# Performance work log

Hardware: AMD Instinct MI355X
Metric: run time of the kernel (lower is better)

The kernel has to match this reference:

```python
import jax, jax.numpy as jnp
import numpy as np

WIN_SIZE = 11
SIGMA = 1.5
WEIGHTS = np.array([0.0448, 0.2856, 0.3001, 0.2363, 0.1333], dtype=np.float32)
K1, K2 = 0.01, 0.03
DATA_RANGE = 255.0
C1 = (K1 * DATA_RANGE) ** 2
C2 = (K2 * DATA_RANGE) ** 2
N_SCALES = 5


def _gauss1d():
    coords = np.arange(WIN_SIZE, dtype=np.float32) - WIN_SIZE // 2
    g = np.exp(-(coords ** 2) / (2.0 * SIGMA ** 2))
    g /= g.sum()
    return jnp.asarray(g, dtype=jnp.float32)


def _blur(x, g):
    # separable depthwise gaussian blur, VALID padding (matches pytorch_msssim)
    C = x.shape[1]
    wh = jnp.tile(g.reshape(1, 1, 1, WIN_SIZE), (C, 1, 1, 1))
    wv = jnp.tile(g.reshape(1, 1, WIN_SIZE, 1), (C, 1, 1, 1))
    dn = ('NCHW', 'OIHW', 'NCHW')
    x = jax.lax.conv_general_dilated(x, wh, (1, 1), 'VALID', dimension_numbers=dn, feature_group_count=C)
    x = jax.lax.conv_general_dilated(x, wv, (1, 1), 'VALID', dimension_numbers=dn, feature_group_count=C)
    return x


def _ssim(X, Y, g):
    mu1 = _blur(X, g)
    mu2 = _blur(Y, g)
    mu1_sq = mu1 * mu1
    mu2_sq = mu2 * mu2
    mu1_mu2 = mu1 * mu2
    sigma1_sq = _blur(X * X, g) - mu1_sq
    sigma2_sq = _blur(Y * Y, g) - mu2_sq
    sigma12 = _blur(X * Y, g) - mu1_mu2
    cs_map = (2.0 * sigma12 + C2) / (sigma1_sq + sigma2_sq + C2)
    ssim_map = ((2.0 * mu1_mu2 + C1) / (mu1_sq + mu2_sq + C1)) * cs_map
    return ssim_map.mean(axis=(2, 3)), cs_map.mean(axis=(2, 3))  # [B,C] each


def _avg_pool2(x):
    # avg_pool2d kernel=2 stride=2; H,W chosen even at every scale so padding=0
    return jax.lax.reduce_window(x, 0.0, jax.lax.add, (1, 1, 2, 2), (1, 1, 2, 2), 'VALID') / 4.0


def setup_inputs() -> dict:
    key = jax.random.key(0)
    k1, k2 = jax.random.split(key)
    shape = (32, 3, 384, 384)
    prediction = jax.random.uniform(k1, shape, dtype=jnp.float32) * DATA_RANGE
    truth = jax.random.uniform(k2, shape, dtype=jnp.float32) * DATA_RANGE
    return {"prediction": prediction, "truth": truth}


def reference(prediction, truth):
    g = _gauss1d()
    w = jnp.asarray(WEIGHTS)
    X, Y = prediction, truth
    mcs = []
    for i in range(N_SCALES):
        ssim_pc, cs = _ssim(X, Y, g)
        if i < N_SCALES - 1:
            mcs.append(jax.nn.relu(cs))
            X = _avg_pool2(X)
            Y = _avg_pool2(Y)
    vals = jnp.stack(mcs + [jax.nn.relu(ssim_pc)], axis=0)  # [5,B,C]
    ms_ssim_val = jnp.prod(vals ** w.reshape(-1, 1, 1), axis=0)  # [B,C]
    return 1.0 - ms_ssim_val.mean()
```

## Files before the change

kernel.cpp:

```cpp
#include <hip/hip_runtime.h>
#include <math.h>


namespace {

constexpr int NIMG = 96;
constexpr float TWO_C1 = 13.005f;
constexpr float TWO_C2 = 117.045f;

__device__ constexpr float GW[11] = {
    0.00102838f, 0.00759875f, 0.03600077f, 0.10936070f, 0.21300553f,
    0.26601172f,
    0.21300553f, 0.10936070f, 0.03600077f, 0.00759875f, 0.00102838f};

typedef float f2 __attribute__((ext_vector_type(2)));
typedef float f4 __attribute__((ext_vector_type(4)));

__device__ __forceinline__ f2 pk_mul(f2 a, f2 b) {
  f2 d;
  asm("v_pk_mul_f32 %0, %1, %2" : "=v"(d) : "v"(a), "v"(b));
  return d;
}
__device__ __forceinline__ f2 pk_mul_s1lo(f2 a, f2 b) {
  f2 d;
  asm("v_pk_mul_f32 %0, %1, %2 op_sel:[0,0] op_sel_hi:[1,0]"
      : "=v"(d) : "v"(a), "v"(b));
  return d;
}
__device__ __forceinline__ void fma_w(f2& d, f2 q, f2 p) {
  asm("v_pk_fma_f32 %0, %1, %2, %0 op_sel:[0,0,0] op_sel_hi:[0,1,1]"
      : "+v"(d) : "v"(q), "v"(p));
}
__device__ __forceinline__ void fma_nl(f2& d, f2 q, f2 t) {
  asm("v_pk_fma_f32 %0, %1, %2, %0 op_sel:[0,0,0] op_sel_hi:[1,0,1]"
      : "+v"(d) : "v"(q), "v"(t));
}
__device__ __forceinline__ void fma_nh(f2& d, f2 q, f2 t) {
  asm("v_pk_fma_f32 %0, %1, %2, %0 op_sel:[0,1,0] op_sel_hi:[1,1,1]"
      : "+v"(d) : "v"(q), "v"(t));
}
__device__ __forceinline__ void fma_sl(f2& d, f2 q, f2 t) {
  asm("v_pk_fma_f32 %0, %1, %2, %0 op_sel:[1,0,0] op_sel_hi:[0,0,1]"
      : "+v"(d) : "v"(q), "v"(t));
}
__device__ __forceinline__ void fma_sh(f2& d, f2 q, f2 t) {
  asm("v_pk_fma_f32 %0, %1, %2, %0 op_sel:[1,1,0] op_sel_hi:[0,1,1]"
      : "+v"(d) : "v"(q), "v"(t));
}

__device__ __forceinline__ float wshl1(float v) {
  return __int_as_float(__builtin_amdgcn_mov_dpp(
      __float_as_int(v), 0x130, 0xF, 0xF, true));
}
__device__ __forceinline__ f2 wshl1v(f2 v) {
  f2 r;
  r.x = wshl1(v.x);
  r.y = wshl1(v.y);
  return r;
}

struct SPtrs {
  const float* x0;
  const float* y0;
  const float* ip[4];
};

template <bool BASE, bool CLAMP>
__device__ __forceinline__ void vblur(const float* __restrict__ XP,
                                      const float* __restrict__ YP, int row0,
                                      int W2, int H, int cp, f2 (&AU)[4],
                                      f2 (&AW)[4], f2 (&BU)[4], f2 (&BW)[4],
                                      const f2 (&QQ)[6]) {
  const f2* PA = (const f2*)XP;
  const f2* PB = (const f2*)YP;
  const f4* PV = (const f4*)XP;
  f2 sa[14], sb[14];
  f4 sv[14];
#pragma unroll
  for (int j = 0; j < 14; ++j) {
    int rin = row0 + j;
    if (CLAMP) rin = rin < H - 1 ? rin : H - 1;
    const int off = rin * W2 + cp;
    if (BASE) {
      sa[j] = PA[off];
      sb[j] = PB[off];
    } else {
      sv[j] = PV[off];
    }
  }
  __builtin_amdgcn_sched_barrier(0);
#pragma unroll
  for (int j = 0; j < 14; ++j) {
    f2 Pu, Pw;
    if (BASE) {
      f2 pa = sa[j], pb = sb[j];
      Pu = pa + pb;
      Pw = pa - pb;
    } else {
      f4 v = sv[j];
      Pu.x = v.x; Pu.y = v.y;
      Pw.x = v.z; Pw.y = v.w;
    }
    f2 Qu = pk_mul(Pu, Pu), Qw = pk_mul(Pw, Pw);
#pragma unroll
    for (int i = 0; i < 4; ++i) {
      const int k = j - i;
      if (k >= 0 && k <= 10) {
        const int qi = k <= 5 ? k : 10 - k;
        fma_w(AU[i], QQ[qi], Pu);
        fma_w(AW[i], QQ[qi], Pw);
        fma_w(BU[i], QQ[qi], Qu);
        fma_w(BW[i], QQ[qi], Qw);
      }
    }
  }
}

__global__ __launch_bounds__(256, 3) void ssim_all(SPtrs sp,
                                                   float* __restrict__ acc) {
  __shared__ float red[2][4];

  const int tile = blockIdx.x;
  int s;
  if (tile < 96) s = 0;
  else if (tile < 120) s = 1;
  else if (tile < 126) s = 2;
  else if (tile < 129) s = 3;
  else s = 4;
  const int tstart[5] = {0, 96, 120, 126, 129};
  const int HH[5] = {384, 192, 96, 48, 24};
  const int NTX[5] = {4, 2, 1, 1, 1};
  const int TWM[5] = {94, 92, 86, 38, 14};
  const int lt = tile - tstart[s];
  const int H = HH[s], W = H, OH = H - 10, OW = W - 10, W2 = W >> 1;
  const int tx = lt % NTX[s], by = lt / NTX[s];
  const int x0 = tx * TWM[s];
  const int tw = (TWM[s] < OW - x0) ? TWM[s] : OW - x0;
  const int img = blockIdx.z;

  const float* XP;
  const float* YP = nullptr;
  if (s == 0) {
    XP = sp.x0 + (size_t)img * 384 * 384;
    YP = sp.y0 + (size_t)img * 384 * 384;
  } else {
    XP = sp.ip[s - 1] + (size_t)img * H * W * 2;
  }

  const int t = threadIdx.x;
  const int lane = t & 63, wv = t >> 6;
  int cp = (x0 >> 1) + lane;
  cp = cp < W2 - 1 ? cp : W2 - 1;
  const int row0 = by * 16 + wv * 4;

  f2 QQ[6];
  QQ[0].x = GW[0]; QQ[0].y = 0.f;
#pragma unroll
  for (int n = 1; n < 6; ++n) { QQ[n].x = GW[n]; QQ[n].y = GW[n - 1]; }

  float ssim_s = 0.f, cs_s = 0.f;

  if (row0 < OH) {
    f2 AU[4] = {}, AW[4] = {}, BU[4] = {}, BW[4] = {};
    const bool noclamp = (row0 + 13 <= H - 1);
    if (s == 0) {
      if (noclamp) vblur<true, false>(XP, YP, row0, W2, H, cp, AU, AW, BU, BW, QQ);
      else         vblur<true, true >(XP, YP, row0, W2, H, cp, AU, AW, BU, BW, QQ);
    } else {
      if (noclamp) vblur<false, false>(XP, YP, row0, W2, H, cp, AU, AW, BU, BW, QQ);
      else         vblur<false, true >(XP, YP, row0, W2, H, cp, AU, AW, BU, BW, QQ);
    }

    auto hb = [&QQ](f2 tt) -> f2 {
      f2 h = pk_mul_s1lo(QQ[0], tt);
      fma_nh(h, QQ[1], tt);
      tt = wshl1v(tt);
      fma_nl(h, QQ[2], tt);
      fma_nh(h, QQ[3], tt);
      tt = wshl1v(tt);
      fma_nl(h, QQ[4], tt);
      fma_nh(h, QQ[5], tt);
      tt = wshl1v(tt);
      fma_sl(h, QQ[5], tt);
      fma_sh(h, QQ[4], tt);
      tt = wshl1v(tt);
      fma_sl(h, QQ[3], tt);
      fma_sh(h, QQ[2], tt);
      tt = wshl1v(tt);
      fma_sl(h, QQ[1], tt);
      fma_sh(h, QQ[0], tt);
      return h;
    };

    const bool vx = (2 * lane) < tw;
    const bool vy = (2 * lane + 1) < tw;
#pragma unroll
    for (int i = 0; i < 4; ++i) {
      if (row0 + i < OH) {
        f2 bU = hb(AU[i]), bW = hb(AW[i]);
        f2 bU2 = hb(BU[i]), bW2 = hb(BW[i]);
        f2 m2u = pk_mul(bU, bU), m2w = pk_mul(bW, bW);
        f2 Pm = m2u - m2w;
        f2 Qm = m2u + m2w;
        f2 Am = bU2 - bW2;
        f2 Bm = bU2 + bW2;
        float csx = (Am.x - Pm.x + TWO_C2) *
                    __builtin_amdgcn_rcpf(Bm.x - Qm.x + TWO_C2);
        float lx = (Pm.x + TWO_C1) * __builtin_amdgcn_rcpf(Qm.x + TWO_C1);
        float csy = (Am.y - Pm.y + TWO_C2) *
                    __builtin_amdgcn_rcpf(Bm.y - Qm.y + TWO_C2);
        float ly = (Pm.y + TWO_C1) * __builtin_amdgcn_rcpf(Qm.y + TWO_C1);
        if (vx) { cs_s += csx; ssim_s += lx * csx; }
        if (vy) { cs_s += csy; ssim_s += ly * csy; }
      }
    }
  }

#pragma unroll
  for (int off = 32; off > 0; off >>= 1) {
    ssim_s += __shfl_down(ssim_s, off);
    cs_s += __shfl_down(cs_s, off);
  }
  if (lane == 0) { red[0][wv] = ssim_s; red[1][wv] = cs_s; }
  __syncthreads();
  if (t == 0) {
    atomicAdd(&acc[(2 * s + 0) * NIMG + img],
              red[0][0] + red[0][1] + red[0][2] + red[0][3]);
    atomicAdd(&acc[(2 * s + 1) * NIMG + img],
              red[1][0] + red[1][1] + red[1][2] + red[1][3]);
  }
}

__global__ __launch_bounds__(256) void pyramid_kernel(
    const float* __restrict__ X, const float* __restrict__ Y,
    float* __restrict__ i1, float* __restrict__ i2,
    float* __restrict__ i3, float* __restrict__ i4,
    float* __restrict__ acc) {
  const int img = blockIdx.y;
  const int t = threadIdx.x;
  if (blockIdx.x == 0 && img == 0) {
    for (int i = t; i < 10 * NIMG; i += 256) acc[i] = 0.f;
  }
  const int wv = t >> 6, lane = t & 63;
  const int tidx = blockIdx.x * 4 + wv;
  const int tx = tidx % 6, ty = tidx / 6;
  const int r = lane >> 4, c = lane & 15;

  const float* Xs = X + (size_t)img * 384 * 384;
  const float* Ys = Y + (size_t)img * 384 * 384;
  f4* p1 = (f4*)i1 + (size_t)img * 192 * 96;
  f4* p2 = (f4*)i2 + (size_t)img * 96 * 48;
  f4* p3 = (f4*)i3 + (size_t)img * 48 * 24;
  f4* p4 = (f4*)i4 + (size_t)img * 24 * 12;

  float h4u = 0.f, h4w = 0.f;
#pragma unroll
  for (int b = 0; b < 2; ++b) {
    const int gr = ty * 16 + b * 8 + 2 * r;
    const int gc = tx * 64 + 4 * c;
    f4 xu = *(const f4*)&Xs[(size_t)gr * 384 + gc];
    f4 xv = *(const f4*)&Xs[(size_t)(gr + 1) * 384 + gc];
    f4 yu = *(const f4*)&Ys[(size_t)gr * 384 + gc];
    f4 yv = *(const f4*)&Ys[(size_t)(gr + 1) * 384 + gc];
    float ax = 0.25f * (xu.x + xu.y + xv.x + xv.y);
    float bx = 0.25f * (xu.z + xu.w + xv.z + xv.w);
    float ay = 0.25f * (yu.x + yu.y + yv.x + yv.y);
    float by = 0.25f * (yu.z + yu.w + yv.z + yv.w);
    float u0 = ax + ay, u1v = bx + by, w0 = ax - ay, w1v = bx - by;
    {
      f4 st; st.x = u0; st.y = u1v; st.z = w0; st.w = w1v;
      p1[(size_t)(ty * 8 + b * 4 + r) * 96 + tx * 16 + c] = st;
    }
    float hu = u0 + u1v, hw = w0 + w1v;
    float su = 0.25f * (hu + __shfl_xor(hu, 16));
    float sw = 0.25f * (hw + __shfl_xor(hw, 16));
    float suh = __shfl_xor(su, 1), swh = __shfl_xor(sw, 1);
    if ((r & 1) == 0 && (c & 1) == 0) {
      f4 st; st.x = su; st.y = suh; st.z = sw; st.w = swh;
      p2[(size_t)(ty * 4 + 2 * b + (r >> 1)) * 48 + tx * 8 + (c >> 1)] = st;
    }
    float au = su + __shfl_xor(su, 1);
    float aw = sw + __shfl_xor(sw, 1);
    float u3 = 0.25f * (au + __shfl_xor(au, 32));
    float w3 = 0.25f * (aw + __shfl_xor(aw, 32));
    float u3h = __shfl_xor(u3, 2), w3h = __shfl_xor(w3, 2);
    if (r == 0 && (c & 3) == 0) {
      f4 st; st.x = u3; st.y = u3h; st.z = w3; st.w = w3h;
      p3[(size_t)(ty * 2 + b) * 24 + tx * 4 + (c >> 2)] = st;
    }
    float hu4 = u3 + __shfl_xor(u3, 2);
    float hw4 = w3 + __shfl_xor(w3, 2);
    if (b == 0) {
      h4u = hu4; h4w = hw4;
    } else {
      float l4u = 0.25f * (h4u + hu4), l4w = 0.25f * (h4w + hw4);
      float l4uh = __shfl_xor(l4u, 4), l4wh = __shfl_xor(l4w, 4);
      if (r == 0 && (c & 7) == 0) {
        f4 st; st.x = l4u; st.y = l4uh; st.z = l4w; st.w = l4wh;
        p4[(size_t)ty * 12 + tx * 2 + (c >> 3)] = st;
      }
    }
  }
}

__global__ void final_kernel(const float* __restrict__ acc,
                             float* __restrict__ out) {
  __shared__ float prods[NIMG];
  const float wts[5] = {0.0448f, 0.2856f, 0.3001f, 0.2363f, 0.1333f};
  const float inv_npix[5] = {1.f / (374.f * 374.f), 1.f / (182.f * 182.f),
                             1.f / (86.f * 86.f),  1.f / (38.f * 38.f),
                             1.f / (14.f * 14.f)};
  int t = threadIdx.x;
  if (t < NIMG) {
    float p = 1.f;
#pragma unroll
    for (int s = 0; s < 5; ++s) {
      float sum = (s < 4) ? acc[(s * 2 + 1) * NIMG + t]
                          : acc[(s * 2 + 0) * NIMG + t];
      float m = sum * inv_npix[s];
      m = m > 0.f ? m : 0.f;
      p *= powf(m, wts[s]);
    }
    prods[t] = p;
  }
  __syncthreads();
  if (t == 0) {
    float s = 0.f;
    for (int i = 0; i < NIMG; ++i) s += prods[i];
    out[0] = 1.f - s / (float)NIMG;
  }
}

}

extern "C" void kernel_launch(void* const* d_in, const int* in_sizes, int n_in,
                              void* d_out, int out_size, void* d_ws,
                              size_t ws_size, hipStream_t stream) {
  const float* X0 = (const float*)d_in[0];
  const float* Y0 = (const float*)d_in[1];
  float* out = (float*)d_out;
  float* ws = (float*)d_ws;

  const size_t L1 = (size_t)NIMG * 192 * 192 * 2;
  const size_t L2 = (size_t)NIMG * 96 * 96 * 2;
  const size_t L3 = (size_t)NIMG * 48 * 48 * 2;
  const size_t L4 = (size_t)NIMG * 24 * 24 * 2;

  float* i1 = ws;
  float* i2 = i1 + L1;
  float* i3 = i2 + L2;
  float* i4 = i3 + L3;
  float* acc = i4 + L4;

  pyramid_kernel<<<dim3(36, NIMG), dim3(256), 0, stream>>>(
      X0, Y0, i1, i2, i3, i4, acc);

  SPtrs sp;
  sp.x0 = X0; sp.y0 = Y0;
  sp.ip[0] = i1; sp.ip[1] = i2; sp.ip[2] = i3; sp.ip[3] = i4;

  ssim_all<<<dim3(130, 1, NIMG), dim3(256), 0, stream>>>(sp, acc);

  final_kernel<<<dim3(1), dim3(128), 0, stream>>>(acc, out);
}
```

Measured before the change: 232.8 us.

## Stage block's input rows in shared memory and raise occupancy target

Each block now cooperatively loads its 26 input rows (the 16-row tile plus the 10-row halo) into LDS as sum/difference pairs once, and each wave reads its 14 rows from LDS. Previously every wave fetched its own 14 rows from global memory, so overlapping halo rows were loaded several times. The launch bound is raised from 3 to 6 blocks per SIMD to improve latency hiding. In exchange this adds a __syncthreads and LDS traffic, and the tighter register budget may cause spills. The pyramid offset expression is also rewritten to an equivalent form.

```diff
diff --git a/kernel.cpp b/kernel.cpp
--- a/kernel.cpp
+++ b/kernel.cpp
@@ -65,59 +65,10 @@
   const float* ip[4];
 };
 
-template <bool BASE, bool CLAMP>
-__device__ __forceinline__ void vblur(const float* __restrict__ XP,
-                                      const float* __restrict__ YP, int row0,
-                                      int W2, int H, int cp, f2 (&AU)[4],
-                                      f2 (&AW)[4], f2 (&BU)[4], f2 (&BW)[4],
-                                      const f2 (&QQ)[6]) {
-  const f2* PA = (const f2*)XP;
-  const f2* PB = (const f2*)YP;
-  const f4* PV = (const f4*)XP;
-  f2 sa[14], sb[14];
-  f4 sv[14];
-#pragma unroll
-  for (int j = 0; j < 14; ++j) {
-    int rin = row0 + j;
-    if (CLAMP) rin = rin < H - 1 ? rin : H - 1;
-    const int off = rin * W2 + cp;
-    if (BASE) {
-      sa[j] = PA[off];
-      sb[j] = PB[off];
-    } else {
-      sv[j] = PV[off];
-    }
-  }
-  __builtin_amdgcn_sched_barrier(0);
-#pragma unroll
-  for (int j = 0; j < 14; ++j) {
-    f2 Pu, Pw;
-    if (BASE) {
-      f2 pa = sa[j], pb = sb[j];
-      Pu = pa + pb;
-      Pw = pa - pb;
-    } else {
-      f4 v = sv[j];
-      Pu.x = v.x; Pu.y = v.y;
-      Pw.x = v.z; Pw.y = v.w;
-    }
-    f2 Qu = pk_mul(Pu, Pu), Qw = pk_mul(Pw, Pw);
-#pragma unroll
-    for (int i = 0; i < 4; ++i) {
-      const int k = j - i;
-      if (k >= 0 && k <= 10) {
-        const int qi = k <= 5 ? k : 10 - k;
-        fma_w(AU[i], QQ[qi], Pu);
-        fma_w(AW[i], QQ[qi], Pw);
-        fma_w(BU[i], QQ[qi], Qu);
-        fma_w(BW[i], QQ[qi], Qw);
-      }
-    }
-  }
-}
-
-__global__ __launch_bounds__(256, 3) void ssim_all(SPtrs sp,
+__global__ __launch_bounds__(256, 6) void ssim_all(SPtrs sp,
                                                    float* __restrict__ acc) {
+  __shared__ f2 SU[26][64];
+  __shared__ f2 SW[26][64];
   __shared__ float red[2][4];
 
   const int tile = blockIdx.x;
@@ -144,14 +95,53 @@
     XP = sp.x0 + (size_t)img * 384 * 384;
     YP = sp.y0 + (size_t)img * 384 * 384;
   } else {
-    XP = sp.ip[s - 1] + (size_t)img * H * W * 2;
+    XP = sp.ip[s - 1] + (size_t)img * H * W2 * 4;
   }
 
   const int t = threadIdx.x;
   const int lane = t & 63, wv = t >> 6;
-  int cp = (x0 >> 1) + lane;
-  cp = cp < W2 - 1 ? cp : W2 - 1;
   const int row0 = by * 16 + wv * 4;
+
+  {
+    const int lc = lane;
+    const int r0 = t >> 6;
+    int gcp = (x0 >> 1) + lc;
+    gcp = gcp < W2 - 1 ? gcp : W2 - 1;
+    const int brow = by * 16;
+    if (s == 0) {
+      const f2* PA = (const f2*)XP;
+      const f2* PB = (const f2*)YP;
+#pragma unroll
+      for (int k = 0; k < 7; ++k) {
+        const int r = r0 + 4 * k;
+        if (r < 26) {
+          int grow = brow + r;
+          grow = grow < H - 1 ? grow : H - 1;
+          const int off = grow * W2 + gcp;
+          f2 pa = PA[off], pb = PB[off];
+          SU[r][lc] = pa + pb;
+          SW[r][lc] = pa - pb;
+        }
+      }
+    } else {
+      const f4* PV = (const f4*)XP;
+#pragma unroll
+      for (int k = 0; k < 7; ++k) {
+        const int r = r0 + 4 * k;
+        if (r < 26) {
+          int grow = brow + r;
+          grow = grow < H - 1 ? grow : H - 1;
+          f4 v = PV[grow * W2 + gcp];
+          f2 u, w;
+          u.x = v.x; u.y = v.y;
+          w.x = v.z; w.y = v.w;
+          SU[r][lc] = u;
+          SW[r][lc] = w;
+        }
+      }
+    }
+  }
+  __syncthreads();
 
   f2 QQ[6];
   QQ[0].x = GW[0]; QQ[0].y = 0.f;
@@ -162,13 +152,22 @@
 
   if (row0 < OH) {
     f2 AU[4] = {}, AW[4] = {}, BU[4] = {}, BW[4] = {};
-    const bool noclamp = (row0 + 13 <= H - 1);
-    if (s == 0) {
-      if (noclamp) vblur<true, false>(XP, YP, row0, W2, H, cp, AU, AW, BU, BW, QQ);
-      else         vblur<true, true >(XP, YP, row0, W2, H, cp, AU, AW, BU, BW, QQ);
-    } else {
-      if (noclamp) vblur<false, false>(XP, YP, row0, W2, H, cp, AU, AW, BU, BW, QQ);
-      else         vblur<false, true >(XP, YP, row0, W2, H, cp, AU, AW, BU, BW, QQ);
+#pragma unroll
+    for (int j = 0; j < 14; ++j) {
+      f2 Pu = SU[wv * 4 + j][lane];
+      f2 Pw = SW[wv * 4 + j][lane];
+      f2 Qu = pk_mul(Pu, Pu), Qw = pk_mul(Pw, Pw);
+#pragma unroll
+      for (int i = 0; i < 4; ++i) {
+        const int k = j - i;
+        if (k >= 0 && k <= 10) {
+          const int qi = k <= 5 ? k : 10 - k;
+          fma_w(AU[i], QQ[qi], Pu);
+          fma_w(AW[i], QQ[qi], Pw);
+          fma_w(BU[i], QQ[qi], Qu);
+          fma_w(BW[i], QQ[qi], Qw);
+        }
+      }
     }
 
     auto hb = [&QQ](f2 tt) -> f2 {
```

New measurement: 233.5 us. About the same (+0.3%).

## Fuse pyramid downsampling with scale-0 SSIM into one kernel launch

Applied to the files above, without the earlier changes.

Scale-0 SSIM tiles depend only on the original inputs, so they are merged into the same grid as the pyramid downsampling blocks and run concurrently. The coarser scales run in a separate kernel afterward. The accumulator zeroing moves to a hipMemsetAsync, and launch bounds rise to 4 blocks per SM. This is meant to overlap pyramid work with the dominant scale-0 work and share reads of X/Y in cache. The costs are an extra memset launch and tighter register limits that could cause spilling.

```diff
diff --git a/kernel.cpp b/kernel.cpp
--- a/kernel.cpp
+++ b/kernel.cpp
@@ -60,8 +60,6 @@
 }
 
 struct SPtrs {
-  const float* x0;
-  const float* y0;
   const float* ip[4];
 };
 
@@ -116,37 +114,14 @@
   }
 }
 
-__global__ __launch_bounds__(256, 3) void ssim_all(SPtrs sp,
-                                                   float* __restrict__ acc) {
+template <bool BASE>
+__device__ __forceinline__ void ssim_tile(const float* __restrict__ XP,
+                                          const float* __restrict__ YP,
+                                          int H, int x0, int tw, int by,
+                                          int s, int img,
+                                          float* __restrict__ acc) {
   __shared__ float red[2][4];
-
-  const int tile = blockIdx.x;
-  int s;
-  if (tile < 96) s = 0;
-  else if (tile < 120) s = 1;
-  else if (tile < 126) s = 2;
-  else if (tile < 129) s = 3;
-  else s = 4;
-  const int tstart[5] = {0, 96, 120, 126, 129};
-  const int HH[5] = {384, 192, 96, 48, 24};
-  const int NTX[5] = {4, 2, 1, 1, 1};
-  const int TWM[5] = {94, 92, 86, 38, 14};
-  const int lt = tile - tstart[s];
-  const int H = HH[s], W = H, OH = H - 10, OW = W - 10, W2 = W >> 1;
-  const int tx = lt % NTX[s], by = lt / NTX[s];
-  const int x0 = tx * TWM[s];
-  const int tw = (TWM[s] < OW - x0) ? TWM[s] : OW - x0;
-  const int img = blockIdx.z;
-
-  const float* XP;
-  const float* YP = nullptr;
-  if (s == 0) {
-    XP = sp.x0 + (size_t)img * 384 * 384;
-    YP = sp.y0 + (size_t)img * 384 * 384;
-  } else {
-    XP = sp.ip[s - 1] + (size_t)img * H * W * 2;
-  }
-
+  const int W2 = H >> 1, OH = H - 10;
   const int t = threadIdx.x;
   const int lane = t & 63, wv = t >> 6;
   int cp = (x0 >> 1) + lane;
@@ -163,13 +138,8 @@
   if (row0 < OH) {
     f2 AU[4] = {}, AW[4] = {}, BU[4] = {}, BW[4] = {};
     const bool noclamp = (row0 + 13 <= H - 1);
-    if (s == 0) {
-      if (noclamp) vblur<true, false>(XP, YP, row0, W2, H, cp, AU, AW, BU, BW, QQ);
-      else         vblur<true, true >(XP, YP, row0, W2, H, cp, AU, AW, BU, BW, QQ);
-    } else {
-      if (noclamp) vblur<false, false>(XP, YP, row0, W2, H, cp, AU, AW, BU, BW, QQ);
-      else         vblur<false, true >(XP, YP, row0, W2, H, cp, AU, AW, BU, BW, QQ);
-    }
+    if (noclamp) vblur<BASE, false>(XP, YP, row0, W2, H, cp, AU, AW, BU, BW, QQ);
+    else         vblur<BASE, true >(XP, YP, row0, W2, H, cp, AU, AW, BU, BW, QQ);
 
     auto hb = [&QQ](f2 tt) -> f2 {
       f2 h = pk_mul_s1lo(QQ[0], tt);
@@ -231,18 +201,13 @@
   }
 }
 
-__global__ __launch_bounds__(256) void pyramid_kernel(
+__device__ __forceinline__ void pyramid_body(
     const float* __restrict__ X, const float* __restrict__ Y,
     float* __restrict__ i1, float* __restrict__ i2,
-    float* __restrict__ i3, float* __restrict__ i4,
-    float* __restrict__ acc) {
-  const int img = blockIdx.y;
+    float* __restrict__ i3, float* __restrict__ i4, int img, int bx) {
   const int t = threadIdx.x;
-  if (blockIdx.x == 0 && img == 0) {
-    for (int i = t; i < 10 * NIMG; i += 256) acc[i] = 0.f;
-  }
   const int wv = t >> 6, lane = t & 63;
-  const int tidx = blockIdx.x * 4 + wv;
+  const int tidx = bx * 4 + wv;
   const int tx = tidx % 6, ty = tidx / 6;
   const int r = lane >> 4, c = lane & 15;
 
@@ -263,10 +228,10 @@
     f4 yu = *(const f4*)&Ys[(size_t)gr * 384 + gc];
     f4 yv = *(const f4*)&Ys[(size_t)(gr + 1) * 384 + gc];
     float ax = 0.25f * (xu.x + xu.y + xv.x + xv.y);
-    float bx = 0.25f * (xu.z + xu.w + xv.z + xv.w);
+    float bx2 = 0.25f * (xu.z + xu.w + xv.z + xv.w);
     float ay = 0.25f * (yu.x + yu.y + yv.x + yv.y);
-    float by = 0.25f * (yu.z + yu.w + yv.z + yv.w);
-    float u0 = ax + ay, u1v = bx + by, w0 = ax - ay, w1v = bx - by;
+    float by2 = 0.25f * (yu.z + yu.w + yv.z + yv.w);
+    float u0 = ax + ay, u1v = bx2 + by2, w0 = ax - ay, w1v = bx2 - by2;
     {
       f4 st; st.x = u0; st.y = u1v; st.z = w0; st.w = w1v;
       p1[(size_t)(ty * 8 + b * 4 + r) * 96 + tx * 16 + c] = st;
@@ -303,6 +268,47 @@
   }
 }
 
+__global__ __launch_bounds__(256, 4) void fused_pyr_s0(
+    const float* __restrict__ X, const float* __restrict__ Y,
+    float* __restrict__ i1, float* __restrict__ i2,
+    float* __restrict__ i3, float* __restrict__ i4,
+    float* __restrict__ acc) {
+  const int img = blockIdx.y;
+  if (blockIdx.x < 36) {
+    pyramid_body(X, Y, i1, i2, i3, i4, img, blockIdx.x);
+    return;
+  }
+  const int lt = blockIdx.x - 36;
+  const int tx = lt & 3, by = lt >> 2;
+  const int x0 = tx * 94;
+  int tw = 374 - x0;
+  tw = tw < 94 ? tw : 94;
+  ssim_tile<true>(X + (size_t)img * 384 * 384, Y + (size_t)img * 384 * 384,
+                  384, x0, tw, by, 0, img, acc);
+}
+
+__global__ __launch_bounds__(256, 4) void ssim_rest(SPtrs sp,
+                                                    float* __restrict__ acc) {
+  const int img = blockIdx.y;
+  const int tile = 96 + blockIdx.x;
+  int s;
+  if (tile < 120) s = 1;
+  else if (tile < 126) s = 2;
+  else if (tile < 129) s = 3;
+  else s = 4;
+  const int tstart[5] = {0, 96, 120, 126, 129};
+  const int HH[5] = {384, 192, 96, 48, 24};
+  const int NTX[5] = {4, 2, 1, 1, 1};
+  const int TWM[5] = {94, 92, 86, 38, 14};
+  const int lt = tile - tstart[s];
+  const int H = HH[s], OW = H - 10;
+  const int tx = lt % NTX[s], by = lt / NTX[s];
+  const int x0 = tx * TWM[s];
+  const int tw = (TWM[s] < OW - x0) ? TWM[s] : OW - x0;
+  const float* XP = sp.ip[s - 1] + (size_t)img * H * (H >> 1) * 4;
+  ssim_tile<false>(XP, nullptr, H, x0, tw, by, s, img, acc);
+}
+
 __global__ void final_kernel(const float* __restrict__ acc,
                              float* __restrict__ out) {
   __shared__ float prods[NIMG];
@@ -352,14 +358,15 @@
   float* i4 = i3 + L3;
   float* acc = i4 + L4;
 
-  pyramid_kernel<<<dim3(36, NIMG), dim3(256), 0, stream>>>(
+  hipMemsetAsync(acc, 0, 10 * NIMG * sizeof(float), stream);
+
+  fused_pyr_s0<<<dim3(36 + 96, NIMG), dim3(256), 0, stream>>>(
       X0, Y0, i1, i2, i3, i4, acc);
 
   SPtrs sp;
-  sp.x0 = X0; sp.y0 = Y0;
   sp.ip[0] = i1; sp.ip[1] = i2; sp.ip[2] = i3; sp.ip[3] = i4;
 
-  ssim_all<<<dim3(130, 1, NIMG), dim3(256), 0, stream>>>(sp, acc);
+  ssim_rest<<<dim3(34, NIMG), dim3(256), 0, stream>>>(sp, acc);
 
   final_kernel<<<dim3(1), dim3(128), 0, stream>>>(acc, out);
 }
```

New measurement: 221.3 us. -4.9%, faster.
